# Kernel tuning notes

Hardware: AMD Instinct MI355X
Metric: run time of the kernel (lower is better)

Reference implementation:

```python
import jax, jax.numpy as jnp
import numpy as np

TAU = 1.0      # gumbel-softmax temperature
ALPHA = 0.05   # mixprop alpha
GDEP = 1       # mixprop depth

B, C, H, W = 16, 512, 96, 96
N = 64  # n_classes / codebook size


def setup_inputs() -> dict:
    key = jax.random.key(0)
    ks = jax.random.split(key, 8)
    u = jax.random.uniform(ks[3], (B, N, H, W), dtype=jnp.float32, minval=1e-6, maxval=1.0 - 1e-6)
    gumbel_noise = -jnp.log(-jnp.log(u))  # standard Gumbel(0,1)
    return {
        "x": jax.random.normal(ks[0], (B, C, H, W), dtype=jnp.float32),
        "centers": jax.random.normal(ks[1], (N, C), dtype=jnp.float32) * 0.1,
        "A": jax.random.uniform(ks[2], (N, N), dtype=jnp.float32),
        "gumbel_noise": gumbel_noise,
        "W_bc": jax.random.normal(ks[4], (1, C), dtype=jnp.float32) * 0.05,
        "b_bc": jnp.zeros((1,), dtype=jnp.float32),
        "W_gcn": jax.random.normal(ks[5], (C, 2 * C), dtype=jnp.float32) * 0.03,
        "b_gcn": jnp.zeros((C,), dtype=jnp.float32),
    }


def _mixprop_centers(centers, A, W_gcn, b_gcn):
    # mixprop on the codebook: centers [N, C] viewed as x of shape [1, C, N, 1]
    n = A.shape[0]
    adj = A + jnp.eye(n, dtype=A.dtype)
    a = adj / adj.sum(axis=1, keepdims=True)           # row-normalized adjacency
    xg = centers.T[None, :, :, None]                    # [1, C, N, 1]
    h = xg
    outs = [h]
    for _ in range(GDEP):
        h = ALPHA * xg + (1.0 - ALPHA) * jnp.einsum('ncwl,vw->ncvl', h, a)
        outs.append(h)
    ho = jnp.concatenate(outs, axis=1)                  # [1, (GDEP+1)*C, N, 1]
    new_c = jnp.einsum('oc,bcvl->bovl', W_gcn, ho) + b_gcn[None, :, None, None]
    return new_c[0, :, :, 0].T                          # [N, C]


def reference(x, centers, A, gumbel_noise, W_bc, b_bc, W_gcn, b_gcn):
    n = centers.shape[0]
    # inner products of features with codebook centers
    inner_products = jnp.einsum('bchw,nc->bnhw', x, centers)          # [B, N, H, W]
    # gumbel-softmax with hard (straight-through) assignment over dim 1
    y = jax.nn.softmax((inner_products + gumbel_noise) / TAU, axis=1)
    hard = jax.nn.one_hot(jnp.argmax(y, axis=1), n, dtype=y.dtype, axis=1)
    one_hot = hard + y - jax.lax.stop_gradient(y)
    # quantized features via codebook gather
    z_q = jnp.einsum('bnhw,nd->bdhw', one_hot, centers)               # [B, C, H, W]
    # 1x1 conv binary classifier + global average pool
    heatmap = jnp.einsum('oc,bchw->bohw', W_bc, z_q) + b_bc[None, :, None, None]  # [B,1,H,W]
    logits = heatmap.mean(axis=(2, 3)).squeeze()                      # [B]
    # graph diffusion of the codebook
    new_centers = _mixprop_centers(centers, A, W_gcn, b_gcn)          # [N, C]
    normed_ip = jnp.einsum('bchw,nc->bnhw', x, new_centers)           # [B, N, H, W]
    cluster_probs = jax.nn.one_hot(jnp.argmax(normed_ip, axis=1), n, dtype=normed_ip.dtype, axis=1)
    cluster_loss = -(cluster_probs * jax.nn.softmax(normed_ip, axis=1)).sum(axis=1).mean()
    return heatmap, logits, cluster_loss, inner_products
```

## Files before the change

kernel.cpp:

```cpp
#include <hip/hip_runtime.h>
#include <math.h>

#define BATCH   16
#define CDIM    512
#define HWDIM   9216
#define NCLS    64
#define TILE    128
#define NTILES  72
#define NCHUNK  16

#define LOGOFF  147456
#define LOSSOFF 147472
#define IPOFF   147473

#define WS_CC   0
#define WS_S    65536
#define WS_PH   65600
#define WS_PC   66752
#define WS_AP   67904

typedef __attribute__((ext_vector_type(8))) short bf16x8;
typedef __attribute__((ext_vector_type(4))) float f32x4;

__device__ __forceinline__ void split3(float v, float& h, float& m, float& l) {
  float hf = __uint_as_float(__float_as_uint(v) & 0xFFFF0000u);
  float r  = v - hf;
  float mf = __uint_as_float(__float_as_uint(r) & 0xFFFF0000u);
  float r2 = r - mf;
  float lf = __uint_as_float(__float_as_uint(r2) & 0xFFFF0000u);
  h = hf; m = mf; l = lf;
}

__device__ __forceinline__ unsigned packbf(float a, float b) {
  return (__float_as_uint(a) >> 16) | (__float_as_uint(b) & 0xFFFF0000u);
}

__device__ __forceinline__ void gl_lds16(const void* g, void* l) {
  __builtin_amdgcn_global_load_lds(
      (const __attribute__((address_space(1))) unsigned int*)g,
      (__attribute__((address_space(3))) unsigned int*)l, 16, 0, 0);
}

__global__ __launch_bounds__(256) void prep_kernel(
    const float* __restrict__ centers, const float* __restrict__ Aadj,
    const float* __restrict__ W_bc, const float* __restrict__ b_bc,
    const float* __restrict__ W_gcn, const float* __restrict__ b_gcn,
    float* __restrict__ ws) {
  __shared__ float c_row[CDIM];
  __shared__ float mix_row[CDIM];
  __shared__ float a_n[NCLS];
  __shared__ float red[256];
  const int n = blockIdx.x;
  const int tid = threadIdx.x;

  for (int c = tid; c < CDIM; c += 256) {
    float v = centers[n * CDIM + c];
    c_row[c] = v;
    ws[WS_CC + n * CDIM + c] = v;
  }
  if (tid < NCLS) a_n[tid] = Aadj[n * NCLS + tid] + (tid == n ? 1.0f : 0.0f);
  __syncthreads();
  if (tid == 0) {
    float ssum = 0.f;
    for (int w = 0; w < NCLS; ++w) ssum += a_n[w];
    red[0] = 1.0f / ssum;
  }
  __syncthreads();
  float inv = red[0];
  if (tid < NCLS) a_n[tid] *= inv;
  __syncthreads();

  for (int c = tid; c < CDIM; c += 256) {
    float acc = 0.f;
    for (int w = 0; w < NCLS; ++w) acc = fmaf(a_n[w], centers[w * CDIM + c], acc);
    mix_row[c] = 0.05f * c_row[c] + 0.95f * acc;
  }
  __syncthreads();

  for (int o = tid; o < CDIM; o += 256) {
    const float4* wr0 = (const float4*)(W_gcn + (size_t)o * 1024);
    const float4* wr1 = (const float4*)(W_gcn + (size_t)o * 1024 + 512);
    float a0 = b_gcn[o], a1 = 0.f, a2 = 0.f, a3 = 0.f;
    #pragma unroll 4
    for (int q = 0; q < 128; ++q) {
      float4 w = wr0[q];
      a0 = fmaf(w.x, c_row[q * 4 + 0], a0);
      a1 = fmaf(w.y, c_row[q * 4 + 1], a1);
      a2 = fmaf(w.z, c_row[q * 4 + 2], a2);
      a3 = fmaf(w.w, c_row[q * 4 + 3], a3);
    }
    #pragma unroll 4
    for (int q = 0; q < 128; ++q) {
      float4 w = wr1[q];
      a0 = fmaf(w.x, mix_row[q * 4 + 0], a0);
      a1 = fmaf(w.y, mix_row[q * 4 + 1], a1);
      a2 = fmaf(w.z, mix_row[q * 4 + 2], a2);
      a3 = fmaf(w.w, mix_row[q * 4 + 3], a3);
    }
    ws[WS_CC + (NCLS + n) * CDIM + o] = (a0 + a1) + (a2 + a3);
  }

  float p = 0.f;
  for (int c = tid; c < CDIM; c += 256) p = fmaf(W_bc[c], c_row[c], p);
  red[tid] = p;
  __syncthreads();
  for (int st = 128; st > 0; st >>= 1) {
    if (tid < st) red[tid] += red[tid + st];
    __syncthreads();
  }
  if (tid == 0) ws[WS_S + n] = red[0] + b_bc[0];
}

__global__ __launch_bounds__(256) void pack_kernel(float* __restrict__ ws) {
  const int gid = blockIdx.x * 256 + threadIdx.x;
  const int lane = gid & 63;
  const int mb = (gid >> 6) & 7;
  const int c = gid >> 9;
  const int row = mb * 16 + (lane & 15);
  const int kb = c * 32 + ((lane >> 4) & 3) * 8;
  const float* src = ws + WS_CC + (size_t)row * CDIM + kb;
  float e[8];
  *(float4*)&e[0] = *(const float4*)(src);
  *(float4*)&e[4] = *(const float4*)(src + 4);
  unsigned dh[4], dm[4], dl[4];
  #pragma unroll
  for (int d = 0; d < 4; ++d) {
    float h0, m0, l0, h1, m1, l1;
    split3(e[2 * d], h0, m0, l0);
    split3(e[2 * d + 1], h1, m1, l1);
    dh[d] = packbf(h0, h1); dm[d] = packbf(m0, m1); dl[d] = packbf(l0, l1);
  }
  const size_t base = WS_AP + (size_t)c * 6144 + (size_t)mb * 256 + (size_t)lane * 4;
  *(uint4*)(ws + base)        = make_uint4(dh[0], dh[1], dh[2], dh[3]);
  *(uint4*)(ws + base + 2048) = make_uint4(dm[0], dm[1], dm[2], dm[3]);
  *(uint4*)(ws + base + 4096) = make_uint4(dl[0], dl[1], dl[2], dl[3]);
}

__global__ __launch_bounds__(256, 3) void main_kernel(
    const float* __restrict__ x, const float* __restrict__ gumbel,
    float* __restrict__ ws, float* __restrict__ out) {
  __shared__ char ldsmem[49152];
  __shared__ float s_sh[NCLS];
  char* ldsA = ldsmem;
  char* ldsB = ldsmem + 24576;

  const int tid = threadIdx.x;
  const int w = tid >> 6, l = tid & 63;
  const int tile = blockIdx.x, b = blockIdx.y;
  const int hw0 = tile * TILE;

  if (tid < NCLS) s_sh[tid] = ws[WS_S + tid];

  const float* xb = x + (size_t)b * CDIM * HWDIM;
  const float* pB = xb + (size_t)(w * 8) * HWDIM + hw0 + l;
  const char* ap = (const char*)(ws + WS_AP);

  f32x4 cip[8], cnp[8];
  #pragma unroll
  for (int i = 0; i < 8; ++i) {
    cip[i] = (f32x4){0.f, 0.f, 0.f, 0.f};
    cnp[i] = (f32x4){0.f, 0.f, 0.f, 0.f};
  }

  float bre[16];

#define STAGE_A(c_) do {                                                      \
    const char* gsrc = ap + (size_t)(c_) * 24576;                             \
    _Pragma("unroll")                                                         \
    for (int i = 0; i < 6; ++i)                                               \
      gl_lds16(gsrc + (i * 256 + tid) * 16, ldsA + (i * 256 + tid) * 16);     \
  } while (0)

#define LOAD_B(c_) do {                                                       \
    const size_t koff = (size_t)(c_) * 32 * HWDIM;                            \
    _Pragma("unroll")                                                         \
    for (int j = 0; j < 8; ++j) {                                             \
      bre[j]     = pB[koff + (size_t)j * HWDIM];                              \
      bre[8 + j] = pB[koff + (size_t)j * HWDIM + 64];                         \
    }                                                                         \
  } while (0)

#define WRITE_B() do {                                                        \
    _Pragma("unroll")                                                         \
    for (int hh = 0; hh < 2; ++hh) {                                          \
      unsigned dh[4], dm[4], dl[4];                                           \
      _Pragma("unroll")                                                       \
      for (int d = 0; d < 4; ++d) {                                           \
        float h0, m0, l0, h1, m1, l1;                                         \
        split3(bre[hh * 8 + 2 * d], h0, m0, l0);                              \
        split3(bre[hh * 8 + 2 * d + 1], h1, m1, l1);                          \
        dh[d] = packbf(h0, h1); dm[d] = packbf(m0, m1); dl[d] = packbf(l0, l1);\
      }                                                                       \
      char* basep = ldsB + ((((l >> 4) + hh * 4) * 64) + (w << 4) + (l & 15)) * 16; \
      *(uint4*)(basep)         = make_uint4(dh[0], dh[1], dh[2], dh[3]);      \
      *(uint4*)(basep + 8192)  = make_uint4(dm[0], dm[1], dm[2], dm[3]);      \
      *(uint4*)(basep + 16384) = make_uint4(dl[0], dl[1], dl[2], dl[3]);      \
    }                                                                         \
  } while (0)

  STAGE_A(0);
  LOAD_B(0);
  WRITE_B();
  __syncthreads();

  for (int c = 0; c < NCHUNK; ++c) {
    if (c < NCHUNK - 1) LOAD_B(c + 1);
    {
      const int la = l * 16;
      bf16x8 aH = *(const bf16x8*)(ldsA + w * 1024 + la);
      bf16x8 aM = *(const bf16x8*)(ldsA + 8192 + w * 1024 + la);
      bf16x8 aL = *(const bf16x8*)(ldsA + 16384 + w * 1024 + la);
      bf16x8 nH = *(const bf16x8*)(ldsA + (4 + w) * 1024 + la);
      bf16x8 nM = *(const bf16x8*)(ldsA + 8192 + (4 + w) * 1024 + la);
      #pragma unroll
      for (int nb = 0; nb < 8; ++nb) {
        bf16x8 bH = *(const bf16x8*)(ldsB + nb * 1024 + la);
        bf16x8 bM = *(const bf16x8*)(ldsB + 8192 + nb * 1024 + la);
        bf16x8 bL = *(const bf16x8*)(ldsB + 16384 + nb * 1024 + la);
        cip[nb] = __builtin_amdgcn_mfma_f32_16x16x32_bf16(aH, bH, cip[nb], 0, 0, 0);
        cip[nb] = __builtin_amdgcn_mfma_f32_16x16x32_bf16(aH, bM, cip[nb], 0, 0, 0);
        cip[nb] = __builtin_amdgcn_mfma_f32_16x16x32_bf16(aM, bH, cip[nb], 0, 0, 0);
        cip[nb] = __builtin_amdgcn_mfma_f32_16x16x32_bf16(aH, bL, cip[nb], 0, 0, 0);
        cip[nb] = __builtin_amdgcn_mfma_f32_16x16x32_bf16(aM, bM, cip[nb], 0, 0, 0);
        cip[nb] = __builtin_amdgcn_mfma_f32_16x16x32_bf16(aL, bH, cip[nb], 0, 0, 0);
        cnp[nb] = __builtin_amdgcn_mfma_f32_16x16x32_bf16(nH, bH, cnp[nb], 0, 0, 0);
        cnp[nb] = __builtin_amdgcn_mfma_f32_16x16x32_bf16(nH, bM, cnp[nb], 0, 0, 0);
        cnp[nb] = __builtin_amdgcn_mfma_f32_16x16x32_bf16(nM, bH, cnp[nb], 0, 0, 0);
      }
    }
    __syncthreads();
    if (c < NCHUNK - 1) {
      STAGE_A(c + 1);
      WRITE_B();
      __syncthreads();
    }
  }

  float* pvv  = (float*)ldsmem;
  int*   pvi  = (int*)(ldsmem + 2048);
  float* pnm  = (float*)(ldsmem + 4096);
  float* pns  = (float*)(ldsmem + 6144);
  float* m2   = (float*)(ldsmem + 8192);
  float* hbuf = (float*)(ldsmem + 8704);
  float* cbuf = (float*)(ldsmem + 9216);

  const size_t bn = (size_t)b * NCLS;
  float* ipo = out + IPOFF;
  const int rbase = 16 * w + (l >> 4) * 4;
  const int c15 = l & 15;

  float bv[8]; int bi[8]; float nm[8];
  #pragma unroll
  for (int nb = 0; nb < 8; ++nb) {
    const int hw = hw0 + nb * 16 + c15;
    float best = -1e30f; int besti = 0;
    #pragma unroll
    for (int r = 0; r < 4; ++r) {
      const int n = rbase + r;
      const float v = cip[nb][r];
      ipo[(bn + n) * HWDIM + hw] = v;
      const float t = v + gumbel[(bn + n) * HWDIM + hw];
      if (t > best) { best = t; besti = n; }
    }
    bv[nb] = best; bi[nb] = besti;
    float m = cnp[nb][0];
    m = fmaxf(m, cnp[nb][1]); m = fmaxf(m, cnp[nb][2]); m = fmaxf(m, cnp[nb][3]);
    nm[nb] = m;
  }
  #pragma unroll
  for (int nb = 0; nb < 8; ++nb) {
    #pragma unroll
    for (int mk = 16; mk <= 32; mk <<= 1) {
      float ov = __shfl_xor(bv[nb], mk);
      int   oi = __shfl_xor(bi[nb], mk);
      if (ov > bv[nb] || (ov == bv[nb] && oi < bi[nb])) { bv[nb] = ov; bi[nb] = oi; }
      nm[nb] = fmaxf(nm[nb], __shfl_xor(nm[nb], mk));
    }
  }
  if ((l >> 4) == 0) {
    #pragma unroll
    for (int nb = 0; nb < 8; ++nb) {
      pvv[w * 128 + nb * 16 + l] = bv[nb];
      pvi[w * 128 + nb * 16 + l] = bi[nb];
      pnm[w * 128 + nb * 16 + l] = nm[nb];
    }
  }
  __syncthreads();

  if (tid < 128) {
    float v = pvv[tid]; int i = pvi[tid];
    #pragma unroll
    for (int ww = 1; ww < 4; ++ww) {
      float v2 = pvv[ww * 128 + tid]; int i2 = pvi[ww * 128 + tid];
      if (v2 > v || (v2 == v && i2 < i)) { v = v2; i = i2; }
    }
    float h = s_sh[i];
    hbuf[tid] = h;
    out[(size_t)b * HWDIM + hw0 + tid] = h;
    float m = pnm[tid];
    #pragma unroll
    for (int ww = 1; ww < 4; ++ww) m = fmaxf(m, pnm[ww * 128 + tid]);
    m2[tid] = m;
  }
  __syncthreads();

  #pragma unroll
  for (int nb = 0; nb < 8; ++nb) {
    const float mm = m2[nb * 16 + c15];
    float s = __expf(cnp[nb][0] - mm) + __expf(cnp[nb][1] - mm)
            + __expf(cnp[nb][2] - mm) + __expf(cnp[nb][3] - mm);
    s += __shfl_xor(s, 16);
    s += __shfl_xor(s, 32);
    if ((l >> 4) == 0) pns[w * 128 + nb * 16 + l] = s;
  }
  __syncthreads();

  if (tid < 128) {
    float S = pns[tid] + pns[128 + tid] + pns[256 + tid] + pns[384 + tid];
    cbuf[tid] = 1.0f / S;
  }
  __syncthreads();

  if (tid < 64) {
    float hs = hbuf[tid] + hbuf[tid + 64];
    float cs = cbuf[tid] + cbuf[tid + 64];
    #pragma unroll
    for (int o = 32; o > 0; o >>= 1) {
      hs += __shfl_down(hs, o);
      cs += __shfl_down(cs, o);
    }
    if (tid == 0) {
      ws[WS_PH + b * NTILES + tile] = hs;
      ws[WS_PC + b * NTILES + tile] = cs;
    }
  }
#undef STAGE_A
#undef LOAD_B
#undef WRITE_B
}

__global__ __launch_bounds__(256) void finish_kernel(
    const float* __restrict__ ws, float* __restrict__ out) {
  __shared__ double sred[256];
  const int tid = threadIdx.x;
  {
    int bb = tid >> 4, lane = tid & 15;
    double s = 0.0;
    for (int t = lane; t < NTILES; t += 16) s += (double)ws[WS_PH + bb * NTILES + t];
    #pragma unroll
    for (int o = 8; o > 0; o >>= 1) s += __shfl_down(s, o, 16);
    if (lane == 0) out[LOGOFF + bb] = (float)(s / (double)HWDIM);
  }
  double c = 0.0;
  for (int i = tid; i < BATCH * NTILES; i += 256) c += (double)ws[WS_PC + i];
  sred[tid] = c;
  __syncthreads();
  for (int st = 128; st > 0; st >>= 1) {
    if (tid < st) sred[tid] += sred[tid + st];
    __syncthreads();
  }
  if (tid == 0) out[LOSSOFF] = (float)(-sred[0] / (double)(BATCH * HWDIM));
}

extern "C" void kernel_launch(void* const* d_in, const int* in_sizes, int n_in,
                              void* d_out, int out_size, void* d_ws, size_t ws_size,
                              hipStream_t stream) {
  const float* x       = (const float*)d_in[0];
  const float* centers = (const float*)d_in[1];
  const float* Aadj    = (const float*)d_in[2];
  const float* gumbel  = (const float*)d_in[3];
  const float* W_bc    = (const float*)d_in[4];
  const float* b_bc    = (const float*)d_in[5];
  const float* W_gcn   = (const float*)d_in[6];
  const float* b_gcn   = (const float*)d_in[7];
  float* out = (float*)d_out;
  float* ws  = (float*)d_ws;

  hipLaunchKernelGGL(prep_kernel, dim3(NCLS), dim3(256), 0, stream,
                     centers, Aadj, W_bc, b_bc, W_gcn, b_gcn, ws);
  hipLaunchKernelGGL(pack_kernel, dim3(32), dim3(256), 0, stream, ws);
  hipLaunchKernelGGL(main_kernel, dim3(NTILES, BATCH), dim3(256), 0, stream,
                     x, gumbel, ws, out);
  hipLaunchKernelGGL(finish_kernel, dim3(1), dim3(256), 0, stream, ws, out);
}
```

Before: 211.0 us.

## Split codebook prep into two kernels and double-buffer main GEMM loop

The old single prep kernel did the W_gcn projection per class row with one thread per output row, re-reading W_gcn in each of 64 blocks. It is now split into prep1 (mixing and the classifier dot product) and prep2, which has 128 blocks that each stage a transposed tile of the concatenated inputs in LDS and produce 4 output channels for all classes. In the main kernel, A fragments are loaded straight from global memory into registers instead of through LDS, and the B tile uses two LDS buffers so each chunk needs one barrier instead of two. This adds an extra kernel launch and more register pressure in the main loop.

Result: faster. 206.3 us (-2.2%).

```diff
diff --git a/kernel.cpp b/kernel.cpp
--- a/kernel.cpp
+++ b/kernel.cpp
@@ -18,6 +18,7 @@
 #define WS_PH   65600
 #define WS_PC   66752
 #define WS_AP   67904
+#define WS_MIX  166208
 
 typedef __attribute__((ext_vector_type(8))) short bf16x8;
 typedef __attribute__((ext_vector_type(4))) float f32x4;
@@ -35,29 +36,15 @@
   return (__float_as_uint(a) >> 16) | (__float_as_uint(b) & 0xFFFF0000u);
 }
 
-__device__ __forceinline__ void gl_lds16(const void* g, void* l) {
-  __builtin_amdgcn_global_load_lds(
-      (const __attribute__((address_space(1))) unsigned int*)g,
-      (__attribute__((address_space(3))) unsigned int*)l, 16, 0, 0);
-}
-
-__global__ __launch_bounds__(256) void prep_kernel(
+__global__ __launch_bounds__(256) void prep1_kernel(
     const float* __restrict__ centers, const float* __restrict__ Aadj,
     const float* __restrict__ W_bc, const float* __restrict__ b_bc,
-    const float* __restrict__ W_gcn, const float* __restrict__ b_gcn,
     float* __restrict__ ws) {
-  __shared__ float c_row[CDIM];
-  __shared__ float mix_row[CDIM];
   __shared__ float a_n[NCLS];
   __shared__ float red[256];
   const int n = blockIdx.x;
   const int tid = threadIdx.x;
 
-  for (int c = tid; c < CDIM; c += 256) {
-    float v = centers[n * CDIM + c];
-    c_row[c] = v;
-    ws[WS_CC + n * CDIM + c] = v;
-  }
   if (tid < NCLS) a_n[tid] = Aadj[n * NCLS + tid] + (tid == n ? 1.0f : 0.0f);
   __syncthreads();
   if (tid == 0) {
@@ -67,41 +54,20 @@
   }
   __syncthreads();
   float inv = red[0];
+  __syncthreads();
   if (tid < NCLS) a_n[tid] *= inv;
   __syncthreads();
 
+  float p = 0.f;
   for (int c = tid; c < CDIM; c += 256) {
+    float v = centers[n * CDIM + c];
+    ws[WS_CC + n * CDIM + c] = v;
     float acc = 0.f;
+    #pragma unroll 8
     for (int w = 0; w < NCLS; ++w) acc = fmaf(a_n[w], centers[w * CDIM + c], acc);
-    mix_row[c] = 0.05f * c_row[c] + 0.95f * acc;
-  }
-  __syncthreads();
-
-  for (int o = tid; o < CDIM; o += 256) {
-    const float4* wr0 = (const float4*)(W_gcn + (size_t)o * 1024);
-    const float4* wr1 = (const float4*)(W_gcn + (size_t)o * 1024 + 512);
-    float a0 = b_gcn[o], a1 = 0.f, a2 = 0.f, a3 = 0.f;
-    #pragma unroll 4
-    for (int q = 0; q < 128; ++q) {
-      float4 w = wr0[q];
-      a0 = fmaf(w.x, c_row[q * 4 + 0], a0);
-      a1 = fmaf(w.y, c_row[q * 4 + 1], a1);
-      a2 = fmaf(w.z, c_row[q * 4 + 2], a2);
-      a3 = fmaf(w.w, c_row[q * 4 + 3], a3);
-    }
-    #pragma unroll 4
-    for (int q = 0; q < 128; ++q) {
-      float4 w = wr1[q];
-      a0 = fmaf(w.x, mix_row[q * 4 + 0], a0);
-      a1 = fmaf(w.y, mix_row[q * 4 + 1], a1);
-      a2 = fmaf(w.z, mix_row[q * 4 + 2], a2);
-      a3 = fmaf(w.w, mix_row[q * 4 + 3], a3);
-    }
-    ws[WS_CC + (NCLS + n) * CDIM + o] = (a0 + a1) + (a2 + a3);
-  }
-
-  float p = 0.f;
-  for (int c = tid; c < CDIM; c += 256) p = fmaf(W_bc[c], c_row[c], p);
+    ws[WS_MIX + n * CDIM + c] = 0.05f * v + 0.95f * acc;
+    p = fmaf(W_bc[c], v, p);
+  }
   red[tid] = p;
   __syncthreads();
   for (int st = 128; st > 0; st >>= 1) {
@@ -109,6 +75,33 @@
     __syncthreads();
   }
   if (tid == 0) ws[WS_S + n] = red[0] + b_bc[0];
+}
+
+__global__ __launch_bounds__(256) void prep2_kernel(
+    const float* __restrict__ W_gcn, const float* __restrict__ b_gcn,
+    float* __restrict__ ws) {
+  __shared__ float catT[128][65];
+  const int tid = threadIdx.x;
+  const int oo = tid >> 6, n = tid & 63;
+  const int o = blockIdx.x * 4 + oo;
+  const float* Wrow = W_gcn + (size_t)o * 1024;
+  float acc = b_gcn[o];
+
+  for (int k0 = 0; k0 < 1024; k0 += 128) {
+    __syncthreads();
+    const float* srcb = (k0 < 512) ? (ws + WS_CC + k0) : (ws + WS_MIX + (k0 - 512));
+    #pragma unroll
+    for (int i = 0; i < 32; ++i) {
+      int idx = i * 256 + tid;
+      int kk = idx & 127, n2 = idx >> 7;
+      catT[kk][n2] = srcb[(size_t)n2 * CDIM + kk];
+    }
+    __syncthreads();
+    #pragma unroll 16
+    for (int kk = 0; kk < 128; ++kk)
+      acc = fmaf(Wrow[k0 + kk], catT[kk][n], acc);
+  }
+  ws[WS_CC + (size_t)(NCLS + n) * CDIM + o] = acc;
 }
 
 __global__ __launch_bounds__(256) void pack_kernel(float* __restrict__ ws) {
@@ -141,8 +134,8 @@
     float* __restrict__ ws, float* __restrict__ out) {
   __shared__ char ldsmem[49152];
   __shared__ float s_sh[NCLS];
-  char* ldsA = ldsmem;
-  char* ldsB = ldsmem + 24576;
+  char* buf0 = ldsmem;
+  char* buf1 = ldsmem + 24576;
 
   const int tid = threadIdx.x;
   const int w = tid >> 6, l = tid & 63;
@@ -163,12 +156,16 @@
   }
 
   float bre[16];
-
-#define STAGE_A(c_) do {                                                      \
-    const char* gsrc = ap + (size_t)(c_) * 24576;                             \
-    _Pragma("unroll")                                                         \
-    for (int i = 0; i < 6; ++i)                                               \
-      gl_lds16(gsrc + (i * 256 + tid) * 16, ldsA + (i * 256 + tid) * 16);     \
+  bf16x8 A0[5], A1[5];
+  const int la16 = l * 16;
+
+#define LOAD_A(AS, c_) do {                                                   \
+    const char* asrc = ap + (size_t)(c_) * 24576;                             \
+    AS[0] = *(const bf16x8*)(asrc + w * 1024 + la16);                         \
+    AS[1] = *(const bf16x8*)(asrc + 8192 + w * 1024 + la16);                  \
+    AS[2] = *(const bf16x8*)(asrc + 16384 + w * 1024 + la16);                 \
+    AS[3] = *(const bf16x8*)(asrc + (4 + w) * 1024 + la16);                   \
+    AS[4] = *(const bf16x8*)(asrc + 8192 + (4 + w) * 1024 + la16);            \
   } while (0)
 
 #define LOAD_B(c_) do {                                                       \
@@ -180,7 +177,7 @@
     }                                                                         \
   } while (0)
 
-#define WRITE_B() do {                                                        \
+#define WRITE_B(WB) do {                                                      \
     _Pragma("unroll")                                                         \
     for (int hh = 0; hh < 2; ++hh) {                                          \
       unsigned dh[4], dm[4], dl[4];                                           \
@@ -191,49 +188,42 @@
         split3(bre[hh * 8 + 2 * d + 1], h1, m1, l1);                          \
         dh[d] = packbf(h0, h1); dm[d] = packbf(m0, m1); dl[d] = packbf(l0, l1);\
       }                                                                       \
-      char* basep = ldsB + ((((l >> 4) + hh * 4) * 64) + (w << 4) + (l & 15)) * 16; \
+      char* basep = (WB) + ((((l >> 4) + hh * 4) * 64) + (w << 4) + (l & 15)) * 16; \
       *(uint4*)(basep)         = make_uint4(dh[0], dh[1], dh[2], dh[3]);      \
       *(uint4*)(basep + 8192)  = make_uint4(dm[0], dm[1], dm[2], dm[3]);      \
       *(uint4*)(basep + 16384) = make_uint4(dl[0], dl[1], dl[2], dl[3]);      \
     }                                                                         \
   } while (0)
 
-  STAGE_A(0);
+#define CHUNK(c_, RB, WB, AC, AN) do {                                        \
+    if ((c_) + 1 < NCHUNK) { LOAD_A(AN, (c_) + 1); LOAD_B((c_) + 1); }        \
+    _Pragma("unroll")                                                         \
+    for (int nb = 0; nb < 8; ++nb) {                                          \
+      bf16x8 bH = *(const bf16x8*)((RB) + nb * 1024 + la16);                  \
+      bf16x8 bM = *(const bf16x8*)((RB) + 8192 + nb * 1024 + la16);           \
+      bf16x8 bL = *(const bf16x8*)((RB) + 16384 + nb * 1024 + la16);          \
+      cip[nb] = __builtin_amdgcn_mfma_f32_16x16x32_bf16(AC[0], bH, cip[nb], 0, 0, 0); \
+      cip[nb] = __builtin_amdgcn_mfma_f32_16x16x32_bf16(AC[0], bM, cip[nb], 0, 0, 0); \
+      cip[nb] = __builtin_amdgcn_mfma_f32_16x16x32_bf16(AC[1], bH, cip[nb], 0, 0, 0); \
+      cip[nb] = __builtin_amdgcn_mfma_f32_16x16x32_bf16(AC[0], bL, cip[nb], 0, 0, 0); \
+      cip[nb] = __builtin_amdgcn_mfma_f32_16x16x32_bf16(AC[1], bM, cip[nb], 0, 0, 0); \
+      cip[nb] = __builtin_amdgcn_mfma_f32_16x16x32_bf16(AC[2], bH, cip[nb], 0, 0, 0); \
+      cnp[nb] = __builtin_amdgcn_mfma_f32_16x16x32_bf16(AC[3], bH, cnp[nb], 0, 0, 0); \
+      cnp[nb] = __builtin_amdgcn_mfma_f32_16x16x32_bf16(AC[3], bM, cnp[nb], 0, 0, 0); \
+      cnp[nb] = __builtin_amdgcn_mfma_f32_16x16x32_bf16(AC[4], bH, cnp[nb], 0, 0, 0); \
+    }                                                                         \
+    if ((c_) + 1 < NCHUNK) WRITE_B(WB);                                       \
+    __syncthreads();                                                          \
+  } while (0)
+
+  LOAD_A(A0, 0);
   LOAD_B(0);
-  WRITE_B();
-  __syncthreads();
-
-  for (int c = 0; c < NCHUNK; ++c) {
-    if (c < NCHUNK - 1) LOAD_B(c + 1);
-    {
-      const int la = l * 16;
-      bf16x8 aH = *(const bf16x8*)(ldsA + w * 1024 + la);
-      bf16x8 aM = *(const bf16x8*)(ldsA + 8192 + w * 1024 + la);
-      bf16x8 aL = *(const bf16x8*)(ldsA + 16384 + w * 1024 + la);
-      bf16x8 nH = *(const bf16x8*)(ldsA + (4 + w) * 1024 + la);
-      bf16x8 nM = *(const bf16x8*)(ldsA + 8192 + (4 + w) * 1024 + la);
-      #pragma unroll
-      for (int nb = 0; nb < 8; ++nb) {
-        bf16x8 bH = *(const bf16x8*)(ldsB + nb * 1024 + la);
-        bf16x8 bM = *(const bf16x8*)(ldsB + 8192 + nb * 1024 + la);
-        bf16x8 bL = *(const bf16x8*)(ldsB + 16384 + nb * 1024 + la);
-        cip[nb] = __builtin_amdgcn_mfma_f32_16x16x32_bf16(aH, bH, cip[nb], 0, 0, 0);
-        cip[nb] = __builtin_amdgcn_mfma_f32_16x16x32_bf16(aH, bM, cip[nb], 0, 0, 0);
-        cip[nb] = __builtin_amdgcn_mfma_f32_16x16x32_bf16(aM, bH, cip[nb], 0, 0, 0);
-        cip[nb] = __builtin_amdgcn_mfma_f32_16x16x32_bf16(aH, bL, cip[nb], 0, 0, 0);
-        cip[nb] = __builtin_amdgcn_mfma_f32_16x16x32_bf16(aM, bM, cip[nb], 0, 0, 0);
-        cip[nb] = __builtin_amdgcn_mfma_f32_16x16x32_bf16(aL, bH, cip[nb], 0, 0, 0);
-        cnp[nb] = __builtin_amdgcn_mfma_f32_16x16x32_bf16(nH, bH, cnp[nb], 0, 0, 0);
-        cnp[nb] = __builtin_amdgcn_mfma_f32_16x16x32_bf16(nH, bM, cnp[nb], 0, 0, 0);
-        cnp[nb] = __builtin_amdgcn_mfma_f32_16x16x32_bf16(nM, bH, cnp[nb], 0, 0, 0);
-      }
-    }
-    __syncthreads();
-    if (c < NCHUNK - 1) {
-      STAGE_A(c + 1);
-      WRITE_B();
-      __syncthreads();
-    }
+  WRITE_B(buf0);
+  __syncthreads();
+
+  for (int cc = 0; cc < NCHUNK; cc += 2) {
+    CHUNK(cc, buf0, buf1, A0, A1);
+    CHUNK(cc + 1, buf1, buf0, A1, A0);
   }
 
   float* pvv  = (float*)ldsmem;
@@ -334,9 +324,10 @@
       ws[WS_PC + b * NTILES + tile] = cs;
     }
   }
-#undef STAGE_A
+#undef LOAD_A
 #undef LOAD_B
 #undef WRITE_B
+#undef CHUNK
 }
 
 __global__ __launch_bounds__(256) void finish_kernel(
@@ -376,8 +367,10 @@
   float* out = (float*)d_out;
   float* ws  = (float*)d_ws;
 
-  hipLaunchKernelGGL(prep_kernel, dim3(NCLS), dim3(256), 0, stream,
-                     centers, Aadj, W_bc, b_bc, W_gcn, b_gcn, ws);
+  hipLaunchKernelGGL(prep1_kernel, dim3(NCLS), dim3(256), 0, stream,
+                     centers, Aadj, W_bc, b_bc, ws);
+  hipLaunchKernelGGL(prep2_kernel, dim3(128), dim3(256), 0, stream,
+                     W_gcn, b_gcn, ws);
   hipLaunchKernelGGL(pack_kernel, dim3(32), dim3(256), 0, stream, ws);
   hipLaunchKernelGGL(main_kernel, dim3(NTILES, BATCH), dim3(256), 0, stream,
                      x, gumbel, ws, out);
```
